# Kernel optimization log

Hardware: AMD Instinct MI355X
Metric: run time of the kernel (lower is better)

Reference implementation:

```python
import jax, jax.numpy as jnp
import numpy as np

D_MODEL = 512
N_HEADS = 8
HEAD_DIM = D_MODEL // N_HEADS
MAX_LEN = 250  # relative table has 2*MAX_LEN-1 = 499 rows
B, L = 2, 2048


def setup_inputs() -> dict:
    rng = jax.random.key(0)
    ks = jax.random.split(rng, 10)
    w = 1.0 / np.sqrt(D_MODEL)
    return {
        "query": jax.random.normal(ks[0], (B, L, D_MODEL), jnp.float32),
        "key": jax.random.normal(ks[1], (B, L, D_MODEL), jnp.float32),
        "value": jax.random.normal(ks[2], (B, L, D_MODEL), jnp.float32),
        "mask": jax.random.randint(ks[3], (B, L), 0, 2, jnp.int32),
        # weights stored as [in, out]; apply as x @ W + b (equivalent to torch Linear)
        "Wq": jax.random.normal(ks[4], (D_MODEL, D_MODEL), jnp.float32) * w,
        "bq": jnp.zeros((D_MODEL,), jnp.float32),
        "Wk": jax.random.normal(ks[5], (D_MODEL, D_MODEL), jnp.float32) * w,
        "bk": jnp.zeros((D_MODEL,), jnp.float32),
        "Wv": jax.random.normal(ks[6], (D_MODEL, D_MODEL), jnp.float32) * w,
        "bv": jnp.zeros((D_MODEL,), jnp.float32),
        "Wo": jax.random.normal(ks[7], (D_MODEL, D_MODEL), jnp.float32) * w,
        "bo": jnp.zeros((D_MODEL,), jnp.float32),
        "rel_table": jax.random.normal(ks[8], (2 * MAX_LEN - 1, HEAD_DIM), jnp.float32),
    }


def reference(query, key, value, mask, Wq, bq, Wk, bk, Wv, bv, Wo, bo, rel_table):
    b, l, d = query.shape
    hd = d // N_HEADS

    def split_heads(x):  # [b,l,d] -> [b,h,l,hd]
        return x.reshape(b, l, N_HEADS, hd).transpose(0, 2, 1, 3)

    Q = split_heads(query @ Wq + bq)
    K = split_heads(key @ Wk + bk)
    V = split_heads(value @ Wv + bv)

    scores = jnp.einsum('bhid,bhjd->bhij', Q, K) / jnp.sqrt(jnp.float32(hd))

    # relative position indices: idx[i,j] = clamp(j - i + MAX_LEN-1, 0, 2*MAX_LEN-2)
    pos = jnp.arange(l)
    idx = jnp.clip(pos[None, :] - pos[:, None] + MAX_LEN - 1, 0, 2 * MAX_LEN - 2)
    rel = rel_table[idx]  # [l, l, hd] gather
    # Shaw-style additive relative-position bias (per-pair scalar from Q . rel)
    scores = scores + jnp.einsum('bhid,ijd->bhij', Q, rel)

    # key-padding mask: [b,l] -> [b,1,1,l]
    scores = jnp.where(mask[:, None, None, :] == 0, jnp.float32(-1e10), scores)

    weights = jax.nn.softmax(scores, axis=-1)  # [b,h,l,l]
    out = jnp.einsum('bhij,bhjd->bhid', weights, V)
    out = out.transpose(0, 2, 1, 3).reshape(b, l, d)
    return out @ Wo + bo
```

## Files before the change

kernel.cpp:

```cpp
#include <hip/hip_runtime.h>
#include <math.h>

#define NREL 499
#define NREL_PAD 500
#define LDB 72
#define LDT 72

typedef __attribute__((ext_vector_type(8))) short bf16x8;
typedef __attribute__((ext_vector_type(4))) float f32x4;

__device__ __forceinline__ float bf2f(ushort x) {
  union { unsigned u; float f; } v; v.u = ((unsigned)x) << 16; return v.f;
}
__device__ __forceinline__ ushort f2bf(float x) {
  union { float f; unsigned u; } v; v.f = x;
  return (ushort)((v.u + 0x8000u) >> 16);
}
__device__ __forceinline__ bf16x8 pack8(float4 a, float4 b) {
  bf16x8 r;
  r[0] = (short)f2bf(a.x); r[1] = (short)f2bf(a.y);
  r[2] = (short)f2bf(a.z); r[3] = (short)f2bf(a.w);
  r[4] = (short)f2bf(b.x); r[5] = (short)f2bf(b.y);
  r[6] = (short)f2bf(b.z); r[7] = (short)f2bf(b.w);
  return r;
}

__global__ __launch_bounds__(256) void prep_wt(const float* __restrict__ W0,
                                               const float* __restrict__ W1,
                                               const float* __restrict__ W2,
                                               const float* __restrict__ W3,
                                               const int* __restrict__ mask,
                                               const float* __restrict__ rel,
                                               ushort* __restrict__ Wt,
                                               ushort* __restrict__ maskbf,
                                               ushort* __restrict__ rel8) {
  __shared__ float T[64][68];
  const int t = threadIdx.x;
  const int k0 = blockIdx.x * 64, n0 = blockIdx.y * 64, z = blockIdx.z;
  const float* W = (z == 0) ? W0 : (z == 1) ? W1 : (z == 2) ? W2 : W3;
#pragma unroll
  for (int s = 0; s < 4; ++s) {
    int idx = t + s * 256;
    int r = idx >> 4, c4 = (idx & 15) << 2;
    *(float4*)&T[r][c4] = *(const float4*)(W + (size_t)(k0 + r) * 512 + n0 + c4);
  }
  if (blockIdx.x == 0 && blockIdx.y == 0) {
    int base = z * 1024 + t * 4;
    int4 mv = *(const int4*)(mask + base);
    ushort4 mo;
    mo.x = mv.x ? 0x3F80 : 0; mo.y = mv.y ? 0x3F80 : 0;
    mo.z = mv.z ? 0x3F80 : 0; mo.w = mv.w ? 0x3F80 : 0;
    *(ushort4*)(maskbf + base) = mo;
  } else if (blockIdx.x == 1 && blockIdx.y == 0) {
    int base = z * 8192 + t * 32;
#pragma unroll
    for (int c = 0; c < 4; ++c) {
      ushort4 o;
      int e0 = base + c * 8;
      ushort tmp[8];
#pragma unroll
      for (int k = 0; k < 8; ++k) {
        int e = e0 + k;
        float v = (e < NREL * 64) ? rel[e] * 8.f : 0.f;
        tmp[k] = f2bf(v);
      }
      *(ushort4*)(rel8 + e0) = make_ushort4(tmp[0], tmp[1], tmp[2], tmp[3]);
      *(ushort4*)(rel8 + e0 + 4) = make_ushort4(tmp[4], tmp[5], tmp[6], tmp[7]);
    }
  }
  __syncthreads();
#pragma unroll
  for (int s = 0; s < 4; ++s) {
    int idx = t + s * 256;
    int row = idx >> 4, c4 = (idx & 15) << 2;
    ushort4 u = make_ushort4(f2bf(T[c4 + 0][row]), f2bf(T[c4 + 1][row]),
                             f2bf(T[c4 + 2][row]), f2bf(T[c4 + 3][row]));
    *(ushort4*)(Wt + (size_t)z * 262144 + (size_t)(n0 + row) * 512 + k0 + c4) = u;
  }
}

template <int MODE, int AFP32>
__device__ __forceinline__ void gemm_tile_body(const void* __restrict__ Av,
                                               const ushort* __restrict__ Wt,
                                               const float* __restrict__ bias,
                                               const int* __restrict__ mvec,
                                               void* __restrict__ outv,
                                               int bx, int by, float oscale) {
  __shared__ ushort As[64 * LDT];
  __shared__ ushort Bs[64 * LDT];
  const int t = threadIdx.x;
  const int lane = t & 63, wave = t >> 6;
  const int m16 = lane & 15, quad = lane >> 4;
  const int koff = quad << 3;
  const int i0 = by * 64, n0 = bx * 64;
  const int row0 = t >> 3, off0 = (t & 7) << 3;
  const int row1 = (t + 256) >> 3, off1 = ((t + 256) & 7) << 3;
  const ushort* Ab16 = (const ushort*)Av + (size_t)i0 * 512;
  const float*  Ab32 = (const float*)Av + (size_t)i0 * 512;
  const ushort* Bb = Wt + (size_t)n0 * 512;

  uint4 ar0, ar1;
  float4 af00, af01, af10, af11;
  if (AFP32) {
    af00 = *(const float4*)(Ab32 + (size_t)row0 * 512 + off0);
    af01 = *(const float4*)(Ab32 + (size_t)row0 * 512 + off0 + 4);
    af10 = *(const float4*)(Ab32 + (size_t)row1 * 512 + off1);
    af11 = *(const float4*)(Ab32 + (size_t)row1 * 512 + off1 + 4);
  } else {
    ar0 = *(const uint4*)(Ab16 + (size_t)row0 * 512 + off0);
    ar1 = *(const uint4*)(Ab16 + (size_t)row1 * 512 + off1);
  }
  uint4 br0 = *(const uint4*)(Bb + (size_t)row0 * 512 + off0);
  uint4 br1 = *(const uint4*)(Bb + (size_t)row1 * 512 + off1);

  f32x4 acc[4] = {{0.f, 0.f, 0.f, 0.f}, {0.f, 0.f, 0.f, 0.f},
                  {0.f, 0.f, 0.f, 0.f}, {0.f, 0.f, 0.f, 0.f}};

  for (int ks = 0; ks < 8; ++ks) {
    __syncthreads();
    if (AFP32) {
      *(bf16x8*)&As[row0 * LDT + off0] = pack8(af00, af01);
      *(bf16x8*)&As[row1 * LDT + off1] = pack8(af10, af11);
    } else {
      *(uint4*)&As[row0 * LDT + off0] = ar0;
      *(uint4*)&As[row1 * LDT + off1] = ar1;
    }
    *(uint4*)&Bs[row0 * LDT + off0] = br0;
    *(uint4*)&Bs[row1 * LDT + off1] = br1;
    __syncthreads();

    const int kn = ((ks + 1) & 7) << 6;
    if (AFP32) {
      af00 = *(const float4*)(Ab32 + (size_t)row0 * 512 + kn + off0);
      af01 = *(const float4*)(Ab32 + (size_t)row0 * 512 + kn + off0 + 4);
      af10 = *(const float4*)(Ab32 + (size_t)row1 * 512 + kn + off1);
      af11 = *(const float4*)(Ab32 + (size_t)row1 * 512 + kn + off1 + 4);
    } else {
      ar0 = *(const uint4*)(Ab16 + (size_t)row0 * 512 + kn + off0);
      ar1 = *(const uint4*)(Ab16 + (size_t)row1 * 512 + kn + off1);
    }
    br0 = *(const uint4*)(Bb + (size_t)row0 * 512 + kn + off0);
    br1 = *(const uint4*)(Bb + (size_t)row1 * 512 + kn + off1);

    __builtin_amdgcn_s_setprio(1);
    if (MODE != 1) {
#pragma unroll
      for (int kh = 0; kh < 2; ++kh) {
        bf16x8 af = *(const bf16x8*)&As[((wave << 4) + m16) * LDT + (kh << 5) + koff];
#pragma unroll
        for (int nt = 0; nt < 4; ++nt) {
          bf16x8 wf = *(const bf16x8*)&Bs[((nt << 4) + m16) * LDT + (kh << 5) + koff];
          acc[nt] = __builtin_amdgcn_mfma_f32_16x16x32_bf16(af, wf, acc[nt], 0, 0, 0);
        }
      }
    } else {
#pragma unroll
      for (int kh = 0; kh < 2; ++kh) {
        bf16x8 wf = *(const bf16x8*)&Bs[((wave << 4) + m16) * LDT + (kh << 5) + koff];
#pragma unroll
        for (int it = 0; it < 4; ++it) {
          bf16x8 af = *(const bf16x8*)&As[((it << 4) + m16) * LDT + (kh << 5) + koff];
          acc[it] = __builtin_amdgcn_mfma_f32_16x16x32_bf16(wf, af, acc[it], 0, 0, 0);
        }
      }
    }
    __builtin_amdgcn_s_setprio(0);
  }

  if (MODE == 0) {
    float* out = (float*)outv;
#pragma unroll
    for (int nt = 0; nt < 4; ++nt) {
      float bn = bias[n0 + (nt << 4) + m16];
#pragma unroll
      for (int r = 0; r < 4; ++r) {
        int i = i0 + (wave << 4) + (quad << 2) + r;
        out[(size_t)i * 512 + n0 + (nt << 4) + m16] = acc[nt][r] + bn;
      }
    }
  } else if (MODE == 2) {
    ushort* out = (ushort*)outv;
    const int b = i0 >> 11, l0 = i0 & 2047, h = n0 >> 6;
#pragma unroll
    for (int nt = 0; nt < 4; ++nt) {
      float bn = bias[n0 + (nt << 4) + m16];
      int d = (nt << 4) + m16;
#pragma unroll
      for (int r = 0; r < 4; ++r) {
        int il = (wave << 4) + (quad << 2) + r;
        out[((size_t)(b * 8 + h) * 2048 + l0 + il) * 64 + d] =
            f2bf((acc[nt][r] + bn) * oscale);
      }
    }
  } else {
    ushort* out = (ushort*)outv;
    const int b = i0 >> 11, l0 = i0 & 2047, h = n0 >> 6;
    float4 b4 = *(const float4*)(bias + n0 + (wave << 4) + (quad << 2));
    float bb[4] = {b4.x, b4.y, b4.z, b4.w};
    float mkf[4];
#pragma unroll
    for (int it = 0; it < 4; ++it)
      mkf[it] = (mvec[b * 2048 + l0 + (it << 4) + m16] != 0) ? 1.f : 0.f;
#pragma unroll
    for (int r = 0; r < 4; ++r) {
      int d = (wave << 4) + (quad << 2) + r;
#pragma unroll
      for (int it = 0; it < 4; ++it) {
        out[((size_t)(b * 8 + h) * 64 + d) * 2048 + l0 + (it << 4) + m16] =
            f2bf((acc[it][r] + bb[r]) * mkf[it]);
      }
    }
  }
}

template <int MODE, int AFP32>
__global__ __launch_bounds__(256) void gemm_tile(const void* __restrict__ A,
                                                 const ushort* __restrict__ Wt,
                                                 const float* __restrict__ bias,
                                                 void* __restrict__ outv) {
  gemm_tile_body<MODE, AFP32>(A, Wt, bias, nullptr, outv, blockIdx.x,
                              blockIdx.y, 1.f);
}

__global__ __launch_bounds__(256) void gemm_qkv(
    const float* __restrict__ q, const float* __restrict__ k,
    const float* __restrict__ v, const ushort* __restrict__ Wt,
    const float* __restrict__ bq, const float* __restrict__ bk,
    const float* __restrict__ bv, const int* __restrict__ mask,
    ushort* __restrict__ Qw, ushort* __restrict__ Kw, ushort* __restrict__ Vtw) {
  const int z = blockIdx.z;
  if (z == 0) {
    gemm_tile_body<2, 1>(q, Wt, bq, nullptr, (void*)Qw, blockIdx.x, blockIdx.y,
                         0.125f);
  } else if (z == 1) {
    gemm_tile_body<2, 1>(k, Wt + 262144, bk, nullptr, (void*)Kw, blockIdx.x,
                         blockIdx.y, 1.f);
  } else {
    gemm_tile_body<1, 1>(v, Wt + 2 * 262144, bv, mask, (void*)Vtw, blockIdx.x,
                         blockIdx.y, 1.f);
  }
}

__global__ __launch_bounds__(256) void qrel_tile(const ushort* __restrict__ Qw,
                                                 const ushort* __restrict__ rel8,
                                                 float* __restrict__ qrel) {
  __shared__ ushort As[64 * LDT];
  __shared__ ushort Bs[64 * LDT];
  const int t = threadIdx.x;
  const int lane = t & 63, wave = t >> 6;
  const int m16 = lane & 15, quad = lane >> 4;
  const int koff = quad << 3;
  const int r0 = blockIdx.x * 64;
  const int i0 = blockIdx.y * 64;
  const int bh = blockIdx.z;
  const int row0 = t >> 3, off0 = (t & 7) << 3;
  const int row1 = (t + 256) >> 3, off1 = ((t + 256) & 7) << 3;

  *(uint4*)&As[row0 * LDT + off0] =
      *(const uint4*)(Qw + ((size_t)bh * 2048 + i0 + row0) * 64 + off0);
  *(uint4*)&As[row1 * LDT + off1] =
      *(const uint4*)(Qw + ((size_t)bh * 2048 + i0 + row1) * 64 + off1);
  *(uint4*)&Bs[row0 * LDT + off0] =
      *(const uint4*)(rel8 + (size_t)(r0 + row0) * 64 + off0);
  *(uint4*)&Bs[row1 * LDT + off1] =
      *(const uint4*)(rel8 + (size_t)(r0 + row1) * 64 + off1);
  __syncthreads();

  f32x4 acc[4] = {{0.f, 0.f, 0.f, 0.f}, {0.f, 0.f, 0.f, 0.f},
                  {0.f, 0.f, 0.f, 0.f}, {0.f, 0.f, 0.f, 0.f}};
#pragma unroll
  for (int kh = 0; kh < 2; ++kh) {
    bf16x8 af = *(const bf16x8*)&As[((wave << 4) + m16) * LDT + (kh << 5) + koff];
#pragma unroll
    for (int nt = 0; nt < 4; ++nt) {
      bf16x8 wf = *(const bf16x8*)&Bs[((nt << 4) + m16) * LDT + (kh << 5) + koff];
      acc[nt] = __builtin_amdgcn_mfma_f32_16x16x32_bf16(af, wf, acc[nt], 0, 0, 0);
    }
  }

#pragma unroll
  for (int nt = 0; nt < 4; ++nt) {
    int r = r0 + (nt << 4) + m16;
    if (r < NREL_PAD) {
#pragma unroll
      for (int rg = 0; rg < 4; ++rg) {
        int i = i0 + (wave << 4) + (quad << 2) + rg;
        qrel[((size_t)bh * 2048 + i) * NREL_PAD + r] = acc[nt][rg];
      }
    }
  }
}

__device__ __forceinline__ void gather_qv(float qv[4][4],
                                          const float* __restrict__ qrow,
                                          float e_lo, float e_hi,
                                          int iq, int iw0, int j0, int quad) {
  if (j0 - iw0 >= 264) {
#pragma unroll
    for (int jt = 0; jt < 4; ++jt)
#pragma unroll
      for (int r = 0; r < 4; ++r) qv[jt][r] = e_hi;
  } else if (iw0 - j0 >= 312) {
#pragma unroll
    for (int jt = 0; jt < 4; ++jt)
#pragma unroll
      for (int r = 0; r < 4; ++r) qv[jt][r] = e_lo;
  } else {
#pragma unroll
    for (int jt = 0; jt < 4; ++jt) {
#pragma unroll
      for (int r = 0; r < 4; ++r) {
        int j = j0 + (jt << 4) + (quad << 2) + r;
        int rr = min(NREL - 1, max(0, j - iq + 249));
        qv[jt][r] = qrow[rr];
      }
    }
  }
}

__global__ __launch_bounds__(256) void flash_attn(
    const ushort* __restrict__ Qw, const ushort* __restrict__ Kw,
    const ushort* __restrict__ Vt, const float* __restrict__ qrel,
    const ushort* __restrict__ maskbf, ushort* __restrict__ attnbf) {
  __shared__ ushort QPs[64 * LDB];
  __shared__ ushort Ks[64 * LDB];
  __shared__ ushort Vs[64 * LDB];
  const int t = threadIdx.x;
  const int lane = t & 63, wave = t >> 6;
  const int m16 = lane & 15, quad = lane >> 4;
  const int koff = quad << 3;
  const int bid = ((int)blockIdx.y << 5) + (int)blockIdx.x;
  const int swz = ((bid & 7) << 6) + (bid >> 3);
  const int i0 = (swz & 31) << 6;
  const int bh = swz >> 5;
  const int b = bh >> 3, h = bh & 7;
  const ushort* Qb = Qw + (size_t)bh * 2048 * 64;
  const ushort* Kb = Kw + (size_t)bh * 2048 * 64;
  const ushort* Vb = Vt + (size_t)bh * 64 * 2048;
  const ushort* mbf = maskbf + b * 2048;
  const int iw0 = i0 + (wave << 4);
  const int iq = iw0 + m16;
  const float* qrow = qrel + ((size_t)bh * 2048 + iq) * NREL_PAD;
  const float e_lo = qrow[0], e_hi = qrow[NREL - 1];

  const int row0 = t >> 3, off0 = (t & 7) << 3;
  const int row1 = (t + 256) >> 3, off1 = ((t + 256) & 7) << 3;

  *(uint4*)&QPs[row0 * LDB + off0] =
      *(const uint4*)(Qb + (size_t)(i0 + row0) * 64 + off0);
  *(uint4*)&QPs[row1 * LDB + off1] =
      *(const uint4*)(Qb + (size_t)(i0 + row1) * 64 + off1);
  __syncthreads();

  bf16x8 qa0 = *(const bf16x8*)&QPs[((wave << 4) + m16) * LDB + koff];
  bf16x8 qa1 = *(const bf16x8*)&QPs[((wave << 4) + m16) * LDB + 32 + koff];

  uint4 kr0 = *(const uint4*)(Kb + (size_t)row0 * 64 + off0);
  uint4 kr1 = *(const uint4*)(Kb + (size_t)row1 * 64 + off1);
  uint4 vr0 = *(const uint4*)(Vb + (size_t)row0 * 2048 + off0);
  uint4 vr1 = *(const uint4*)(Vb + (size_t)row1 * 2048 + off1);
  bf16x8 mfr0 = *(const bf16x8*)(mbf + koff);
  bf16x8 mfr1 = *(const bf16x8*)(mbf + 32 + koff);
  float qv[4][4];
  gather_qv(qv, qrow, e_lo, e_hi, iq, iw0, 0, quad);

  float m_i = -INFINITY;
  f32x4 oacc[4];
  f32x4 lacc = {0.f, 0.f, 0.f, 0.f};
#pragma unroll
  for (int dt = 0; dt < 4; ++dt) oacc[dt] = (f32x4){0.f, 0.f, 0.f, 0.f};

  for (int j0 = 0; j0 < 2048; j0 += 64) {
    __syncthreads();
    *(uint4*)&Ks[row0 * LDB + off0] = kr0;
    *(uint4*)&Ks[row1 * LDB + off1] = kr1;
    *(uint4*)&Vs[row0 * LDB + off0] = vr0;
    *(uint4*)&Vs[row1 * LDB + off1] = vr1;
    __syncthreads();

    const int jn = (j0 + 64) & 2047;
    uint4 kn0 = *(const uint4*)(Kb + (size_t)(jn + row0) * 64 + off0);
    uint4 kn1 = *(const uint4*)(Kb + (size_t)(jn + row1) * 64 + off1);
    uint4 vn0 = *(const uint4*)(Vb + (size_t)row0 * 2048 + jn + off0);
    uint4 vn1 = *(const uint4*)(Vb + (size_t)row1 * 2048 + jn + off1);
    bf16x8 mfn0 = *(const bf16x8*)(mbf + jn + koff);
    bf16x8 mfn1 = *(const bf16x8*)(mbf + jn + 32 + koff);
    float qn[4][4];
    gather_qv(qn, qrow, e_lo, e_hi, iq, iw0, jn, quad);

    f32x4 sacc[4];
    __builtin_amdgcn_s_setprio(1);
#pragma unroll
    for (int jt = 0; jt < 4; ++jt) {
      bf16x8 kb0 = *(const bf16x8*)&Ks[((jt << 4) + m16) * LDB + koff];
      bf16x8 kb1 = *(const bf16x8*)&Ks[((jt << 4) + m16) * LDB + 32 + koff];
      f32x4 z = {qv[jt][0], qv[jt][1], qv[jt][2], qv[jt][3]};
      z = __builtin_amdgcn_mfma_f32_16x16x32_bf16(kb0, qa0, z, 0, 0, 0);
      z = __builtin_amdgcn_mfma_f32_16x16x32_bf16(kb1, qa1, z, 0, 0, 0);
      sacc[jt] = z;
    }
    __builtin_amdgcn_s_setprio(0);

    float t0 = fmaxf(fmaxf(sacc[0][0], sacc[0][1]), fmaxf(sacc[0][2], sacc[0][3]));
    float t1 = fmaxf(fmaxf(sacc[1][0], sacc[1][1]), fmaxf(sacc[1][2], sacc[1][3]));
    float t2 = fmaxf(fmaxf(sacc[2][0], sacc[2][1]), fmaxf(sacc[2][2], sacc[2][3]));
    float t3 = fmaxf(fmaxf(sacc[3][0], sacc[3][1]), fmaxf(sacc[3][2], sacc[3][3]));
    float mx = fmaxf(fmaxf(t0, t1), fmaxf(t2, t3));
    mx = fmaxf(mx, __shfl_xor(mx, 16));
    mx = fmaxf(mx, __shfl_xor(mx, 32));

    if (__any(mx > m_i + 8.f)) {
      float mnew = fmaxf(m_i, mx);
      float al = __expf(m_i - mnew);
      m_i = mnew;
#pragma unroll
      for (int dt = 0; dt < 4; ++dt)
#pragma unroll
        for (int r = 0; r < 4; ++r) oacc[dt][r] *= al;
#pragma unroll
      for (int r = 0; r < 4; ++r) lacc[r] *= al;
    }

    const int prow = ((wave << 4) + m16) * LDB;
#pragma unroll
    for (int jt = 0; jt < 4; ++jt) {
      ushort4 pk;
      pk.x = f2bf(__expf(sacc[jt][0] - m_i));
      pk.y = f2bf(__expf(sacc[jt][1] - m_i));
      pk.z = f2bf(__expf(sacc[jt][2] - m_i));
      pk.w = f2bf(__expf(sacc[jt][3] - m_i));
      *(ushort4*)&QPs[prow + (jt << 4) + (quad << 2)] = pk;
    }
    __asm__ volatile("s_waitcnt lgkmcnt(0)" ::: "memory");

    bf16x8 pa0 = *(const bf16x8*)&QPs[prow + koff];
    bf16x8 pa1 = *(const bf16x8*)&QPs[prow + 32 + koff];
    __builtin_amdgcn_s_setprio(1);
    lacc = __builtin_amdgcn_mfma_f32_16x16x32_bf16(mfr0, pa0, lacc, 0, 0, 0);
    lacc = __builtin_amdgcn_mfma_f32_16x16x32_bf16(mfr1, pa1, lacc, 0, 0, 0);
#pragma unroll
    for (int dt = 0; dt < 4; ++dt) {
      bf16x8 vb0 = *(const bf16x8*)&Vs[((dt << 4) + m16) * LDB + koff];
      bf16x8 vb1 = *(const bf16x8*)&Vs[((dt << 4) + m16) * LDB + 32 + koff];
      oacc[dt] = __builtin_amdgcn_mfma_f32_16x16x32_bf16(vb0, pa0, oacc[dt], 0, 0, 0);
      oacc[dt] = __builtin_amdgcn_mfma_f32_16x16x32_bf16(vb1, pa1, oacc[dt], 0, 0, 0);
    }
    __builtin_amdgcn_s_setprio(0);

    kr0 = kn0; kr1 = kn1; vr0 = vn0; vr1 = vn1;
    mfr0 = mfn0; mfr1 = mfn1;
#pragma unroll
    for (int jt = 0; jt < 4; ++jt)
#pragma unroll
      for (int r = 0; r < 4; ++r) qv[jt][r] = qn[jt][r];
  }

  float inv = 1.0f / lacc[0];
  ushort* dst = attnbf + (size_t)(b * 2048 + iq) * 512 + h * 64;
#pragma unroll
  for (int dt = 0; dt < 4; ++dt) {
    ushort4 st;
    st.x = f2bf(oacc[dt][0] * inv);
    st.y = f2bf(oacc[dt][1] * inv);
    st.z = f2bf(oacc[dt][2] * inv);
    st.w = f2bf(oacc[dt][3] * inv);
    *(ushort4*)(dst + (dt << 4) + (quad << 2)) = st;
  }
}

extern "C" void kernel_launch(void* const* d_in, const int* in_sizes, int n_in,
                              void* d_out, int out_size, void* d_ws,
                              size_t ws_size, hipStream_t stream) {
  const float* query = (const float*)d_in[0];
  const float* key   = (const float*)d_in[1];
  const float* value = (const float*)d_in[2];
  const int*   mask  = (const int*)d_in[3];
  const float* Wq = (const float*)d_in[4];
  const float* bq = (const float*)d_in[5];
  const float* Wk = (const float*)d_in[6];
  const float* bk = (const float*)d_in[7];
  const float* Wv = (const float*)d_in[8];
  const float* bv = (const float*)d_in[9];
  const float* Wo = (const float*)d_in[10];
  const float* bo = (const float*)d_in[11];
  const float* rel = (const float*)d_in[12];

  char* w = (char*)d_ws;
  size_t off = 0;
  ushort* Qw  = (ushort*)(w + off); off += (size_t)16 * 2048 * 64 * 2;
  ushort* Kw  = (ushort*)(w + off); off += (size_t)16 * 2048 * 64 * 2;
  ushort* Vtw = (ushort*)(w + off); off += (size_t)16 * 64 * 2048 * 2;
  ushort* Wt  = (ushort*)(w + off); off += (size_t)4 * 512 * 512 * 2;
  float* qrel = (float*)(w + off);  off += (size_t)16 * 2048 * NREL_PAD * 4;
  ushort* attnbf = (ushort*)(w + off); off += (size_t)4096 * 512 * 2;
  ushort* maskbf = (ushort*)(w + off); off += (size_t)2 * 2048 * 2;
  ushort* rel8 = (ushort*)(w + off); off += (size_t)512 * 64 * 2;
  float* out = (float*)d_out;

  dim3 bb(256);
  hipLaunchKernelGGL(prep_wt, dim3(8, 8, 4), bb, 0, stream, Wq, Wk, Wv, Wo,
                     mask, rel, Wt, maskbf, rel8);
  hipLaunchKernelGGL(gemm_qkv, dim3(8, 64, 3), bb, 0, stream, query, key, value,
                     Wt, bq, bk, bv, mask, Qw, Kw, Vtw);
  hipLaunchKernelGGL(qrel_tile, dim3(8, 32, 16), bb, 0, stream, Qw, rel8, qrel);
  hipLaunchKernelGGL(flash_attn, dim3(32, 16), bb, 0, stream, Qw, Kw, Vtw, qrel,
                     maskbf, attnbf);
  hipLaunchKernelGGL((gemm_tile<0, 0>), dim3(8, 64), bb, 0, stream, attnbf,
                     Wt + 3 * 262144, bo, (void*)out);
}
```

Before: 219.1 us.

## Store relative-position scores as fp16 and unroll flash loop with ping-pong registers

The Q·rel intermediate table moves from fp32 to fp16. This halves the bytes qrel_tile writes and flash_attn gathers (16×2048×500 entries). The flash-attention main loop is also manually unrolled by two, alternating register sets A/B for the prefetched K/V/mask/qrel values, so the copies between next-tile and current-tile registers go away. The cost is lower precision in the additive bias, plus higher register pressure and code size from the macro-expanded unroll.

```diff
diff --git a/kernel.cpp b/kernel.cpp
--- a/kernel.cpp
+++ b/kernel.cpp
@@ -15,6 +15,12 @@
 __device__ __forceinline__ ushort f2bf(float x) {
   union { float f; unsigned u; } v; v.f = x;
   return (ushort)((v.u + 0x8000u) >> 16);
+}
+__device__ __forceinline__ ushort f2h(float x) {
+  union { _Float16 h; ushort u; } v; v.h = (_Float16)x; return v.u;
+}
+__device__ __forceinline__ float h2f(ushort u) {
+  union { _Float16 h; ushort u; } v; v.u = u; return (float)v.h;
 }
 __device__ __forceinline__ bf16x8 pack8(float4 a, float4 b) {
   bf16x8 r;
@@ -55,7 +61,6 @@
     int base = z * 8192 + t * 32;
 #pragma unroll
     for (int c = 0; c < 4; ++c) {
-      ushort4 o;
       int e0 = base + c * 8;
       ushort tmp[8];
 #pragma unroll
@@ -243,7 +248,7 @@
 
 __global__ __launch_bounds__(256) void qrel_tile(const ushort* __restrict__ Qw,
                                                  const ushort* __restrict__ rel8,
-                                                 float* __restrict__ qrel) {
+                                                 ushort* __restrict__ qrelh) {
   __shared__ ushort As[64 * LDT];
   __shared__ ushort Bs[64 * LDT];
   const int t = threadIdx.x;
@@ -285,14 +290,14 @@
 #pragma unroll
       for (int rg = 0; rg < 4; ++rg) {
         int i = i0 + (wave << 4) + (quad << 2) + rg;
-        qrel[((size_t)bh * 2048 + i) * NREL_PAD + r] = acc[nt][rg];
+        qrelh[((size_t)bh * 2048 + i) * NREL_PAD + r] = f2h(acc[nt][rg]);
       }
     }
   }
 }
 
 __device__ __forceinline__ void gather_qv(float qv[4][4],
-                                          const float* __restrict__ qrow,
+                                          const ushort* __restrict__ qrow,
                                           float e_lo, float e_hi,
                                           int iq, int iw0, int j0, int quad) {
   if (j0 - iw0 >= 264) {
@@ -312,7 +317,7 @@
       for (int r = 0; r < 4; ++r) {
         int j = j0 + (jt << 4) + (quad << 2) + r;
         int rr = min(NREL - 1, max(0, j - iq + 249));
-        qv[jt][r] = qrow[rr];
+        qv[jt][r] = h2f(qrow[rr]);
       }
     }
   }
@@ -320,7 +325,7 @@
 
 __global__ __launch_bounds__(256) void flash_attn(
     const ushort* __restrict__ Qw, const ushort* __restrict__ Kw,
-    const ushort* __restrict__ Vt, const float* __restrict__ qrel,
+    const ushort* __restrict__ Vt, const ushort* __restrict__ qrelh,
     const ushort* __restrict__ maskbf, ushort* __restrict__ attnbf) {
   __shared__ ushort QPs[64 * LDB];
   __shared__ ushort Ks[64 * LDB];
@@ -340,8 +345,8 @@
   const ushort* mbf = maskbf + b * 2048;
   const int iw0 = i0 + (wave << 4);
   const int iq = iw0 + m16;
-  const float* qrow = qrel + ((size_t)bh * 2048 + iq) * NREL_PAD;
-  const float e_lo = qrow[0], e_hi = qrow[NREL - 1];
+  const ushort* qrow = qrelh + ((size_t)bh * 2048 + iq) * NREL_PAD;
+  const float e_lo = h2f(qrow[0]), e_hi = h2f(qrow[NREL - 1]);
 
   const int row0 = t >> 3, off0 = (t & 7) << 3;
   const int row1 = (t + 256) >> 3, off1 = ((t + 256) & 7) << 3;
@@ -355,105 +360,109 @@
   bf16x8 qa0 = *(const bf16x8*)&QPs[((wave << 4) + m16) * LDB + koff];
   bf16x8 qa1 = *(const bf16x8*)&QPs[((wave << 4) + m16) * LDB + 32 + koff];
 
-  uint4 kr0 = *(const uint4*)(Kb + (size_t)row0 * 64 + off0);
-  uint4 kr1 = *(const uint4*)(Kb + (size_t)row1 * 64 + off1);
-  uint4 vr0 = *(const uint4*)(Vb + (size_t)row0 * 2048 + off0);
-  uint4 vr1 = *(const uint4*)(Vb + (size_t)row1 * 2048 + off1);
-  bf16x8 mfr0 = *(const bf16x8*)(mbf + koff);
-  bf16x8 mfr1 = *(const bf16x8*)(mbf + 32 + koff);
-  float qv[4][4];
-  gather_qv(qv, qrow, e_lo, e_hi, iq, iw0, 0, quad);
-
   float m_i = -INFINITY;
   f32x4 oacc[4];
   f32x4 lacc = {0.f, 0.f, 0.f, 0.f};
 #pragma unroll
   for (int dt = 0; dt < 4; ++dt) oacc[dt] = (f32x4){0.f, 0.f, 0.f, 0.f};
 
-  for (int j0 = 0; j0 < 2048; j0 += 64) {
-    __syncthreads();
-    *(uint4*)&Ks[row0 * LDB + off0] = kr0;
-    *(uint4*)&Ks[row1 * LDB + off1] = kr1;
-    *(uint4*)&Vs[row0 * LDB + off0] = vr0;
-    *(uint4*)&Vs[row1 * LDB + off1] = vr1;
-    __syncthreads();
-
-    const int jn = (j0 + 64) & 2047;
-    uint4 kn0 = *(const uint4*)(Kb + (size_t)(jn + row0) * 64 + off0);
-    uint4 kn1 = *(const uint4*)(Kb + (size_t)(jn + row1) * 64 + off1);
-    uint4 vn0 = *(const uint4*)(Vb + (size_t)row0 * 2048 + jn + off0);
-    uint4 vn1 = *(const uint4*)(Vb + (size_t)row1 * 2048 + jn + off1);
-    bf16x8 mfn0 = *(const bf16x8*)(mbf + jn + koff);
-    bf16x8 mfn1 = *(const bf16x8*)(mbf + jn + 32 + koff);
-    float qn[4][4];
-    gather_qv(qn, qrow, e_lo, e_hi, iq, iw0, jn, quad);
-
-    f32x4 sacc[4];
-    __builtin_amdgcn_s_setprio(1);
-#pragma unroll
-    for (int jt = 0; jt < 4; ++jt) {
-      bf16x8 kb0 = *(const bf16x8*)&Ks[((jt << 4) + m16) * LDB + koff];
-      bf16x8 kb1 = *(const bf16x8*)&Ks[((jt << 4) + m16) * LDB + 32 + koff];
-      f32x4 z = {qv[jt][0], qv[jt][1], qv[jt][2], qv[jt][3]};
-      z = __builtin_amdgcn_mfma_f32_16x16x32_bf16(kb0, qa0, z, 0, 0, 0);
-      z = __builtin_amdgcn_mfma_f32_16x16x32_bf16(kb1, qa1, z, 0, 0, 0);
-      sacc[jt] = z;
-    }
-    __builtin_amdgcn_s_setprio(0);
-
-    float t0 = fmaxf(fmaxf(sacc[0][0], sacc[0][1]), fmaxf(sacc[0][2], sacc[0][3]));
-    float t1 = fmaxf(fmaxf(sacc[1][0], sacc[1][1]), fmaxf(sacc[1][2], sacc[1][3]));
-    float t2 = fmaxf(fmaxf(sacc[2][0], sacc[2][1]), fmaxf(sacc[2][2], sacc[2][3]));
-    float t3 = fmaxf(fmaxf(sacc[3][0], sacc[3][1]), fmaxf(sacc[3][2], sacc[3][3]));
-    float mx = fmaxf(fmaxf(t0, t1), fmaxf(t2, t3));
-    mx = fmaxf(mx, __shfl_xor(mx, 16));
-    mx = fmaxf(mx, __shfl_xor(mx, 32));
-
-    if (__any(mx > m_i + 8.f)) {
-      float mnew = fmaxf(m_i, mx);
-      float al = __expf(m_i - mnew);
-      m_i = mnew;
-#pragma unroll
-      for (int dt = 0; dt < 4; ++dt)
-#pragma unroll
-        for (int r = 0; r < 4; ++r) oacc[dt][r] *= al;
-#pragma unroll
-      for (int r = 0; r < 4; ++r) lacc[r] *= al;
-    }
-
-    const int prow = ((wave << 4) + m16) * LDB;
-#pragma unroll
-    for (int jt = 0; jt < 4; ++jt) {
-      ushort4 pk;
-      pk.x = f2bf(__expf(sacc[jt][0] - m_i));
-      pk.y = f2bf(__expf(sacc[jt][1] - m_i));
-      pk.z = f2bf(__expf(sacc[jt][2] - m_i));
-      pk.w = f2bf(__expf(sacc[jt][3] - m_i));
-      *(ushort4*)&QPs[prow + (jt << 4) + (quad << 2)] = pk;
-    }
-    __asm__ volatile("s_waitcnt lgkmcnt(0)" ::: "memory");
-
-    bf16x8 pa0 = *(const bf16x8*)&QPs[prow + koff];
-    bf16x8 pa1 = *(const bf16x8*)&QPs[prow + 32 + koff];
-    __builtin_amdgcn_s_setprio(1);
-    lacc = __builtin_amdgcn_mfma_f32_16x16x32_bf16(mfr0, pa0, lacc, 0, 0, 0);
-    lacc = __builtin_amdgcn_mfma_f32_16x16x32_bf16(mfr1, pa1, lacc, 0, 0, 0);
-#pragma unroll
-    for (int dt = 0; dt < 4; ++dt) {
-      bf16x8 vb0 = *(const bf16x8*)&Vs[((dt << 4) + m16) * LDB + koff];
-      bf16x8 vb1 = *(const bf16x8*)&Vs[((dt << 4) + m16) * LDB + 32 + koff];
-      oacc[dt] = __builtin_amdgcn_mfma_f32_16x16x32_bf16(vb0, pa0, oacc[dt], 0, 0, 0);
-      oacc[dt] = __builtin_amdgcn_mfma_f32_16x16x32_bf16(vb1, pa1, oacc[dt], 0, 0, 0);
-    }
-    __builtin_amdgcn_s_setprio(0);
-
-    kr0 = kn0; kr1 = kn1; vr0 = vn0; vr1 = vn1;
-    mfr0 = mfn0; mfr1 = mfn1;
-#pragma unroll
-    for (int jt = 0; jt < 4; ++jt)
-#pragma unroll
-      for (int r = 0; r < 4; ++r) qv[jt][r] = qn[jt][r];
-  }
+  uint4 krA0 = *(const uint4*)(Kb + (size_t)row0 * 64 + off0);
+  uint4 krA1 = *(const uint4*)(Kb + (size_t)row1 * 64 + off1);
+  uint4 vrA0 = *(const uint4*)(Vb + (size_t)row0 * 2048 + off0);
+  uint4 vrA1 = *(const uint4*)(Vb + (size_t)row1 * 2048 + off1);
+  bf16x8 mfA0 = *(const bf16x8*)(mbf + koff);
+  bf16x8 mfA1 = *(const bf16x8*)(mbf + 32 + koff);
+  float qvA[4][4];
+  gather_qv(qvA, qrow, e_lo, e_hi, iq, iw0, 0, quad);
+  uint4 krB0, krB1, vrB0, vrB1;
+  bf16x8 mfB0, mfB1;
+  float qvB[4][4];
+
+#define FLASH_STEP(KR0, KR1, VR0, VR1, MF0, MF1, QV,                          \
+                   KN0, KN1, VN0, VN1, MG0, MG1, QN, JN)                      \
+  do {                                                                        \
+    __syncthreads();                                                          \
+    *(uint4*)&Ks[row0 * LDB + off0] = KR0;                                    \
+    *(uint4*)&Ks[row1 * LDB + off1] = KR1;                                    \
+    *(uint4*)&Vs[row0 * LDB + off0] = VR0;                                    \
+    *(uint4*)&Vs[row1 * LDB + off1] = VR1;                                    \
+    __syncthreads();                                                          \
+    KN0 = *(const uint4*)(Kb + (size_t)((JN) + row0) * 64 + off0);            \
+    KN1 = *(const uint4*)(Kb + (size_t)((JN) + row1) * 64 + off1);            \
+    VN0 = *(const uint4*)(Vb + (size_t)row0 * 2048 + (JN) + off0);            \
+    VN1 = *(const uint4*)(Vb + (size_t)row1 * 2048 + (JN) + off1);            \
+    MG0 = *(const bf16x8*)(mbf + (JN) + koff);                                \
+    MG1 = *(const bf16x8*)(mbf + (JN) + 32 + koff);                           \
+    gather_qv(QN, qrow, e_lo, e_hi, iq, iw0, (JN), quad);                     \
+    f32x4 sacc[4];                                                            \
+    __builtin_amdgcn_s_setprio(1);                                            \
+    _Pragma("unroll")                                                         \
+    for (int jt = 0; jt < 4; ++jt) {                                          \
+      bf16x8 kf0 = *(const bf16x8*)&Ks[((jt << 4) + m16) * LDB + koff];       \
+      bf16x8 kf1 = *(const bf16x8*)&Ks[((jt << 4) + m16) * LDB + 32 + koff];  \
+      f32x4 z = {QV[jt][0], QV[jt][1], QV[jt][2], QV[jt][3]};                 \
+      z = __builtin_amdgcn_mfma_f32_16x16x32_bf16(kf0, qa0, z, 0, 0, 0);      \
+      z = __builtin_amdgcn_mfma_f32_16x16x32_bf16(kf1, qa1, z, 0, 0, 0);      \
+      sacc[jt] = z;                                                           \
+    }                                                                         \
+    __builtin_amdgcn_s_setprio(0);                                            \
+    float t0 = fmaxf(fmaxf(sacc[0][0], sacc[0][1]),                           \
+                     fmaxf(sacc[0][2], sacc[0][3]));                          \
+    float t1 = fmaxf(fmaxf(sacc[1][0], sacc[1][1]),                           \
+                     fmaxf(sacc[1][2], sacc[1][3]));                          \
+    float t2 = fmaxf(fmaxf(sacc[2][0], sacc[2][1]),                           \
+                     fmaxf(sacc[2][2], sacc[2][3]));                          \
+    float t3 = fmaxf(fmaxf(sacc[3][0], sacc[3][1]),                           \
+                     fmaxf(sacc[3][2], sacc[3][3]));                          \
+    float mx = fmaxf(fmaxf(t0, t1), fmaxf(t2, t3));                           \
+    mx = fmaxf(mx, __shfl_xor(mx, 16));                                       \
+    mx = fmaxf(mx, __shfl_xor(mx, 32));                                       \
+    if (__any(mx > m_i + 8.f)) {                                              \
+      float mnew = fmaxf(m_i, mx);                                            \
+      float al = __expf(m_i - mnew);                                          \
+      m_i = mnew;                                                             \
+      _Pragma("unroll")                                                       \
+      for (int dt = 0; dt < 4; ++dt) {                                        \
+        oacc[dt][0] *= al; oacc[dt][1] *= al;                                 \
+        oacc[dt][2] *= al; oacc[dt][3] *= al;                                 \
+      }                                                                       \
+      lacc[0] *= al; lacc[1] *= al; lacc[2] *= al; lacc[3] *= al;             \
+    }                                                                         \
+    const int prow = ((wave << 4) + m16) * LDB;                               \
+    _Pragma("unroll")                                                         \
+    for (int jt = 0; jt < 4; ++jt) {                                          \
+      ushort4 pk;                                                             \
+      pk.x = f2bf(__expf(sacc[jt][0] - m_i));                                 \
+      pk.y = f2bf(__expf(sacc[jt][1] - m_i));                                 \
+      pk.z = f2bf(__expf(sacc[jt][2] - m_i));                                 \
+      pk.w = f2bf(__expf(sacc[jt][3] - m_i));                                 \
+      *(ushort4*)&QPs[prow + (jt << 4) + (quad << 2)] = pk;                   \
+    }                                                                         \
+    __asm__ volatile("s_waitcnt lgkmcnt(0)" ::: "memory");                    \
+    bf16x8 pa0 = *(const bf16x8*)&QPs[prow + koff];                           \
+    bf16x8 pa1 = *(const bf16x8*)&QPs[prow + 32 + koff];                      \
+    __builtin_amdgcn_s_setprio(1);                                            \
+    lacc = __builtin_amdgcn_mfma_f32_16x16x32_bf16(MF0, pa0, lacc, 0, 0, 0);  \
+    lacc = __builtin_amdgcn_mfma_f32_16x16x32_bf16(MF1, pa1, lacc, 0, 0, 0);  \
+    _Pragma("unroll")                                                         \
+    for (int dt = 0; dt < 4; ++dt) {                                          \
+      bf16x8 vf0 = *(const bf16x8*)&Vs[((dt << 4) + m16) * LDB + koff];       \
+      bf16x8 vf1 = *(const bf16x8*)&Vs[((dt << 4) + m16) * LDB + 32 + koff];  \
+      oacc[dt] =                                                              \
+          __builtin_amdgcn_mfma_f32_16x16x32_bf16(vf0, pa0, oacc[dt], 0, 0, 0); \
+      oacc[dt] =                                                              \
+          __builtin_amdgcn_mfma_f32_16x16x32_bf16(vf1, pa1, oacc[dt], 0, 0, 0); \
+    }                                                                         \
+    __builtin_amdgcn_s_setprio(0);                                            \
+  } while (0)
+
+  for (int j0 = 0; j0 < 2048; j0 += 128) {
+    FLASH_STEP(krA0, krA1, vrA0, vrA1, mfA0, mfA1, qvA,
+               krB0, krB1, vrB0, vrB1, mfB0, mfB1, qvB, j0 + 64);
+    FLASH_STEP(krB0, krB1, vrB0, vrB1, mfB0, mfB1, qvB,
+               krA0, krA1, vrA0, vrA1, mfA0, mfA1, qvA, (j0 + 128) & 2047);
+  }
+#undef FLASH_STEP
 
   float inv = 1.0f / lacc[0];
   ushort* dst = attnbf + (size_t)(b * 2048 + iq) * 512 + h * 64;
@@ -491,7 +500,7 @@
   ushort* Kw  = (ushort*)(w + off); off += (size_t)16 * 2048 * 64 * 2;
   ushort* Vtw = (ushort*)(w + off); off += (size_t)16 * 64 * 2048 * 2;
   ushort* Wt  = (ushort*)(w + off); off += (size_t)4 * 512 * 512 * 2;
-  float* qrel = (float*)(w + off);  off += (size_t)16 * 2048 * NREL_PAD * 4;
+  ushort* qrelh = (ushort*)(w + off); off += (size_t)16 * 2048 * NREL_PAD * 2;
   ushort* attnbf = (ushort*)(w + off); off += (size_t)4096 * 512 * 2;
   ushort* maskbf = (ushort*)(w + off); off += (size_t)2 * 2048 * 2;
   ushort* rel8 = (ushort*)(w + off); off += (size_t)512 * 64 * 2;
@@ -502,9 +511,9 @@
                      mask, rel, Wt, maskbf, rel8);
   hipLaunchKernelGGL(gemm_qkv, dim3(8, 64, 3), bb, 0, stream, query, key, value,
                      Wt, bq, bk, bv, mask, Qw, Kw, Vtw);
-  hipLaunchKernelGGL(qrel_tile, dim3(8, 32, 16), bb, 0, stream, Qw, rel8, qrel);
-  hipLaunchKernelGGL(flash_attn, dim3(32, 16), bb, 0, stream, Qw, Kw, Vtw, qrel,
-                     maskbf, attnbf);
+  hipLaunchKernelGGL(qrel_tile, dim3(8, 32, 16), bb, 0, stream, Qw, rel8, qrelh);
+  hipLaunchKernelGGL(flash_attn, dim3(32, 16), bb, 0, stream, Qw, Kw, Vtw,
+                     qrelh, maskbf, attnbf);
   hipLaunchKernelGGL((gemm_tile<0, 0>), dim3(8, 64), bb, 0, stream, attnbf,
                      Wt + 3 * 262144, bo, (void*)out);
 }
```

New measurement: 212.7 us. -2.9%, faster.
